# Kernel tuning notes

Measured on AMD Instinct MI355X. Metric: run time of the kernel, lower is better.

Reference implementation:

```python
import jax, jax.numpy as jnp
import numpy as np

D_MODEL = 256
NUM_ITEMS = 16
TOPK = 4
TAU = 0.1
EPS = 1e-12  # torch F.normalize eps


def _l2norm(x):
    n = jnp.sqrt(jnp.sum(x * x, axis=-1, keepdims=True))
    return x / jnp.maximum(n, EPS)


def setup_inputs() -> dict:
    key = jax.random.key(0)
    kq, km = jax.random.split(key)
    queries = jax.random.normal(kq, (32, 4096, D_MODEL), dtype=jnp.float32)
    memory = jax.random.normal(km, (NUM_ITEMS, D_MODEL), dtype=jnp.float32)
    memory = _l2norm(memory)  # init normalizes the bank to unit vectors
    return {"queries": queries, "memory": memory}


def reference(queries, memory):
    # queries: [B, Np, d]; memory: [M, d]
    q = _l2norm(queries)
    m = _l2norm(memory)
    sim = jnp.einsum('bnd,md->bnm', q, m) / TAU            # [B, Np, M]
    topk_sim, topk_idx = jax.lax.top_k(sim, TOPK)          # [B, Np, k]
    topk_w = jax.nn.softmax(topk_sim, axis=-1)             # [B, Np, k]
    mem_sel = memory[topk_idx]                             # [B, Np, k, d] (raw memory, matching torch)
    retrieved = jnp.einsum('bnk,bnkd->bnd', topk_w, mem_sel)
    sim_max = jnp.max(sim, axis=-1, keepdims=True)         # [B, Np, 1]
    return retrieved, sim_max
```

## Files before the change

### kernel.cpp

```cpp
#include <hip/hip_runtime.h>
#include <math.h>

#define D 256
#define M 16
#define TAU 0.1f
#define EPSN 1e-12f
#define MEM_STRIDE 260
#define NWAVES 4
#define BATCH 16
#define ROWS_PER_BLOCK (NWAVES * BATCH)

template <int CTRL, int ROW_MASK, int BANK_MASK>
__device__ __forceinline__ float dpp_add(float x) {
    int xi = __builtin_bit_cast(int, x);
    int mi = __builtin_amdgcn_update_dpp(0, xi, CTRL, ROW_MASK, BANK_MASK, true);
    return x + __builtin_bit_cast(float, mi);
}
__device__ __forceinline__ float wave_sum(float x) {
    x = dpp_add<0x111, 0xf, 0xf>(x);
    x = dpp_add<0x112, 0xf, 0xf>(x);
    x = dpp_add<0x114, 0xf, 0xe>(x);
    x = dpp_add<0x118, 0xf, 0xc>(x);
    x = dpp_add<0x142, 0xa, 0xf>(x);
    x = dpp_add<0x143, 0xc, 0xf>(x);
    int t = __builtin_amdgcn_readlane(__builtin_bit_cast(int, x), 63);
    return __builtin_bit_cast(float, t);
}

__global__ __launch_bounds__(256, 4)
void epm_kernel(const float* __restrict__ q, const float* __restrict__ mem,
                float* __restrict__ ret_out, float* __restrict__ smax_out)
{
    __shared__ __align__(16) float mem_lds[M * MEM_STRIDE];
    __shared__ float inv_nm_lds[M];
    __shared__ __align__(16) float qbuf[NWAVES][4 * 68];
    __shared__ float simbuf[NWAVES][M * 17];
    __shared__ float nbuf[NWAVES][BATCH];
    __shared__ __align__(16) float wbuf[NWAVES][BATCH * 4];
    __shared__ int   mbuf[NWAVES][BATCH];

    const int tid  = threadIdx.x;
    const int wv   = tid >> 6;
    const int lane = tid & 63;
    const int m    = lane & 15;
    const int c    = lane >> 4;

    {
        const float4* m4 = (const float4*)mem;
        #pragma unroll
        for (int p = 0; p < 4; ++p) {
            int vi  = p * 256 + tid;
            int row = vi >> 6;
            int col = (vi & 63) * 4;
            float4 v = m4[vi];
            *(float4*)&mem_lds[row * MEM_STRIDE + col] = v;
        }
    }
    __syncthreads();

    if (tid < M) {
        const float4* r4 = (const float4*)&mem_lds[tid * MEM_STRIDE];
        float ss = 0.f;
        #pragma unroll
        for (int j = 0; j < D / 4; ++j) {
            float4 v = r4[j];
            ss += v.x * v.x + v.y * v.y + v.z * v.z + v.w * v.w;
        }
        inv_nm_lds[tid] = 1.0f / fmaxf(sqrtf(ss), EPSN);
    }
    __syncthreads();

    float4 memr[16];
    {
        const float4* src = (const float4*)&mem_lds[m * MEM_STRIDE + c * 64];
        #pragma unroll
        for (int j = 0; j < 16; ++j) memr[j] = src[j];
    }
    const float scale_m = inv_nm_lds[m] * (1.0f / TAU);

    const int wave_row0 = blockIdx.x * ROWS_PER_BLOCK + wv * BATCH;
    float* myq = &qbuf[wv][0];
    float* simw = &simbuf[wv][0];

    float4 qv = ((const float4*)q)[(size_t)wave_row0 * 64 + lane];
    #pragma unroll
    for (int r = 0; r < BATCH; ++r) {
        float4 qn = qv;
        if (r + 1 < BATCH)
            qn = ((const float4*)q)[(size_t)(wave_row0 + r + 1) * 64 + lane];

        float sq = qv.x * qv.x + qv.y * qv.y + qv.z * qv.z + qv.w * qv.w;
        float ss = wave_sum(sq);
        if (lane == 0) nbuf[wv][r] = ss;

        *(float4*)&myq[(lane >> 4) * 68 + (lane & 15) * 4] = qv;

        float acc = 0.f;
        const float4* qs = (const float4*)&myq[c * 68];
        #pragma unroll
        for (int j = 0; j < 16; ++j) {
            float4 a = qs[j];
            float4 b = memr[j];
            acc += a.x * b.x + a.y * b.y + a.z * b.z + a.w * b.w;
        }
        acc += __shfl_xor(acc, 16);
        acc += __shfl_xor(acc, 32);
        if (c == 0) simw[m * 17 + r] = acc * scale_m;
        qv = qn;
    }

    if (lane < BATCH) {
        const int r = lane;
        float ssq = nbuf[wv][r];
        float inv_nq = 1.0f / fmaxf(sqrtf(ssq), EPSN);

        float k0 = -INFINITY, k1 = -INFINITY, k2 = -INFINITY, k3 = -INFINITY;
        #pragma unroll
        for (int mm = 0; mm < M; ++mm) {
            float s = simw[mm * 17 + r] * inv_nq;
            int si = (__builtin_bit_cast(int, s) & ~15) | (15 - mm);
            float ks = __builtin_bit_cast(float, si);
            bool g0 = ks > k0, g1 = ks > k1, g2 = ks > k2, g3 = ks > k3;
            float n3 = g2 ? k2 : (g3 ? ks : k3);
            float n2 = g1 ? k1 : (g2 ? ks : k2);
            float n1 = g0 ? k0 : (g1 ? ks : k1);
            float n0 = g0 ? ks : k0;
            k0 = n0; k1 = n1; k2 = n2; k3 = n3;
        }
        int m0 = 15 - (__builtin_bit_cast(int, k0) & 15);
        int m1 = 15 - (__builtin_bit_cast(int, k1) & 15);
        int m2 = 15 - (__builtin_bit_cast(int, k2) & 15);
        int m3 = 15 - (__builtin_bit_cast(int, k3) & 15);

        float w0 = 1.0f;
        float w1 = __expf(k1 - k0);
        float w2 = __expf(k2 - k0);
        float w3 = __expf(k3 - k0);
        float invd = 1.0f / (w0 + w1 + w2 + w3);

        *(float4*)&wbuf[wv][r * 4] = make_float4(w0 * invd, w1 * invd, w2 * invd, w3 * invd);
        mbuf[wv][r] = m0 | (m1 << 8) | (m2 << 16) | (m3 << 24);

        smax_out[wave_row0 + r] = k0;
    }

    #pragma unroll
    for (int r = 0; r < BATCH; ++r) {
        float4 w = *(const float4*)&wbuf[wv][r * 4];
        int mp = mbuf[wv][r];
        float4 accv = make_float4(0.f, 0.f, 0.f, 0.f);
        #pragma unroll
        for (int k = 0; k < 4; ++k) {
            int mk = (mp >> (8 * k)) & 15;
            float wk = (k == 0) ? w.x : (k == 1) ? w.y : (k == 2) ? w.z : w.w;
            float4 mv = *(const float4*)&mem_lds[mk * MEM_STRIDE + 4 * lane];
            accv.x += wk * mv.x; accv.y += wk * mv.y;
            accv.z += wk * mv.z; accv.w += wk * mv.w;
        }
        ((float4*)ret_out)[(size_t)(wave_row0 + r) * 64 + lane] = accv;
    }
}

extern "C" void kernel_launch(void* const* d_in, const int* in_sizes, int n_in,
                              void* d_out, int out_size, void* d_ws, size_t ws_size,
                              hipStream_t stream) {
    const float* queries = (const float*)d_in[0];
    const float* memory  = (const float*)d_in[1];
    float* out = (float*)d_out;

    const int rows = in_sizes[0] / D;
    float* ret_out  = out;
    float* smax_out = out + (size_t)rows * D;

    const int blocks = rows / ROWS_PER_BLOCK;
    epm_kernel<<<blocks, 64 * NWAVES, 0, stream>>>(queries, memory, ret_out, smax_out);
}
```

Baseline: 241.7 us.

## Compute similarities with per-lane memory slices and butterfly mux reduction

Each lane now holds a 4-float slice of all 16 memory rows in registers and computes partial dot products for all items, then reduces them with a transpose-style butterfly shuffle (mux_reduce), dropping the LDS staging of each query. Memory norms are computed the same way instead of by a 16-thread serial loop, which removes one block barrier. The query prefetch depth goes from 1 to 4 rows. This trades LDS traffic and barriers for more shuffles and register pressure (16 float4 plus 4 prefetched float4).

```diff
diff --git a/kernel.cpp b/kernel.cpp
--- a/kernel.cpp
+++ b/kernel.cpp
@@ -3,12 +3,17 @@
 
 #define D 256
 #define M 16
-#define TAU 0.1f
+#define INV_TAU 10.0f
 #define EPSN 1e-12f
 #define MEM_STRIDE 260
 #define NWAVES 4
 #define BATCH 16
 #define ROWS_PER_BLOCK (NWAVES * BATCH)
+#define SIMW_STRIDE 20
+
+__device__ __forceinline__ float dot4(float4 a, float4 b) {
+    return a.x * b.x + a.y * b.y + a.z * b.z + a.w * b.w;
+}
 
 template <int CTRL, int ROW_MASK, int BANK_MASK>
 __device__ __forceinline__ float dpp_add(float x) {
@@ -27,14 +32,52 @@
     return __builtin_bit_cast(float, t);
 }
 
+__device__ __forceinline__ float mux_reduce(float vals[16], int lane) {
+    {
+        const bool b = (lane & 1) != 0;
+        #pragma unroll
+        for (int j = 0; j < 8; ++j) {
+            float send = b ? vals[j] : vals[j + 8];
+            float recv = __shfl_xor(send, 1);
+            vals[j] = (b ? vals[j + 8] : vals[j]) + recv;
+        }
+    }
+    {
+        const bool b = (lane & 2) != 0;
+        #pragma unroll
+        for (int j = 0; j < 4; ++j) {
+            float send = b ? vals[j] : vals[j + 4];
+            float recv = __shfl_xor(send, 2);
+            vals[j] = (b ? vals[j + 4] : vals[j]) + recv;
+        }
+    }
+    {
+        const bool b = (lane & 4) != 0;
+        #pragma unroll
+        for (int j = 0; j < 2; ++j) {
+            float send = b ? vals[j] : vals[j + 2];
+            float recv = __shfl_xor(send, 4);
+            vals[j] = (b ? vals[j + 2] : vals[j]) + recv;
+        }
+    }
+    {
+        const bool b = (lane & 8) != 0;
+        float send = b ? vals[0] : vals[1];
+        float recv = __shfl_xor(send, 8);
+        vals[0] = (b ? vals[1] : vals[0]) + recv;
+    }
+    float v = vals[0];
+    v += __shfl_xor(v, 16);
+    v += __shfl_xor(v, 32);
+    return v;
+}
+
 __global__ __launch_bounds__(256, 4)
 void epm_kernel(const float* __restrict__ q, const float* __restrict__ mem,
                 float* __restrict__ ret_out, float* __restrict__ smax_out)
 {
     __shared__ __align__(16) float mem_lds[M * MEM_STRIDE];
-    __shared__ float inv_nm_lds[M];
-    __shared__ __align__(16) float qbuf[NWAVES][4 * 68];
-    __shared__ float simbuf[NWAVES][M * 17];
+    __shared__ __align__(16) float simbuf[NWAVES][BATCH * SIMW_STRIDE];
     __shared__ float nbuf[NWAVES][BATCH];
     __shared__ __align__(16) float wbuf[NWAVES][BATCH * 4];
     __shared__ int   mbuf[NWAVES][BATCH];
@@ -42,8 +85,11 @@
     const int tid  = threadIdx.x;
     const int wv   = tid >> 6;
     const int lane = tid & 63;
-    const int m    = lane & 15;
-    const int c    = lane >> 4;
+
+    float4 memr2[16];
+    #pragma unroll
+    for (int m = 0; m < M; ++m)
+        memr2[m] = *(const float4*)&mem[m * D + 4 * lane];
 
     {
         const float4* m4 = (const float4*)mem;
@@ -58,55 +104,43 @@
     }
     __syncthreads();
 
-    if (tid < M) {
-        const float4* r4 = (const float4*)&mem_lds[tid * MEM_STRIDE];
-        float ss = 0.f;
-        #pragma unroll
-        for (int j = 0; j < D / 4; ++j) {
-            float4 v = r4[j];
-            ss += v.x * v.x + v.y * v.y + v.z * v.z + v.w * v.w;
-        }
-        inv_nm_lds[tid] = 1.0f / fmaxf(sqrtf(ss), EPSN);
-    }
-    __syncthreads();
-
-    float4 memr[16];
-    {
-        const float4* src = (const float4*)&mem_lds[m * MEM_STRIDE + c * 64];
-        #pragma unroll
-        for (int j = 0; j < 16; ++j) memr[j] = src[j];
-    }
-    const float scale_m = inv_nm_lds[m] * (1.0f / TAU);
+    float invm_l;
+    {
+        float nmv[16];
+        #pragma unroll
+        for (int m = 0; m < M; ++m) nmv[m] = dot4(memr2[m], memr2[m]);
+        float nm = mux_reduce(nmv, lane);
+        invm_l = 1.0f / fmaxf(sqrtf(nm), EPSN);
+    }
+
+    const int brl = ((lane & 1) << 3) | ((lane & 2) << 1)
+                  | ((lane & 4) >> 1) | ((lane & 8) >> 3);
 
     const int wave_row0 = blockIdx.x * ROWS_PER_BLOCK + wv * BATCH;
-    float* myq = &qbuf[wv][0];
     float* simw = &simbuf[wv][0];
-
-    float4 qv = ((const float4*)q)[(size_t)wave_row0 * 64 + lane];
+    const float4* q4 = (const float4*)q;
+
+    float4 qpre[4];
+    #pragma unroll
+    for (int r = 0; r < 4; ++r)
+        qpre[r] = q4[(size_t)(wave_row0 + r) * 64 + lane];
+
     #pragma unroll
     for (int r = 0; r < BATCH; ++r) {
-        float4 qn = qv;
-        if (r + 1 < BATCH)
-            qn = ((const float4*)q)[(size_t)(wave_row0 + r + 1) * 64 + lane];
-
-        float sq = qv.x * qv.x + qv.y * qv.y + qv.z * qv.z + qv.w * qv.w;
-        float ss = wave_sum(sq);
-        if (lane == 0) nbuf[wv][r] = ss;
-
-        *(float4*)&myq[(lane >> 4) * 68 + (lane & 15) * 4] = qv;
-
-        float acc = 0.f;
-        const float4* qs = (const float4*)&myq[c * 68];
-        #pragma unroll
-        for (int j = 0; j < 16; ++j) {
-            float4 a = qs[j];
-            float4 b = memr[j];
-            acc += a.x * b.x + a.y * b.y + a.z * b.z + a.w * b.w;
-        }
-        acc += __shfl_xor(acc, 16);
-        acc += __shfl_xor(acc, 32);
-        if (c == 0) simw[m * 17 + r] = acc * scale_m;
-        qv = qn;
+        float4 qv = qpre[r & 3];
+        if (r + 4 < BATCH)
+            qpre[r & 3] = q4[(size_t)(wave_row0 + r + 4) * 64 + lane];
+
+        float sq = wave_sum(dot4(qv, qv));
+        if (lane == 0) nbuf[wv][r] = sq;
+
+        float vals[16];
+        #pragma unroll
+        for (int m = 0; m < M; ++m) vals[m] = dot4(qv, memr2[m]);
+
+        float v = mux_reduce(vals, lane);
+
+        if (lane < 16) simw[r * SIMW_STRIDE + brl] = v * invm_l * INV_TAU;
     }
 
     if (lane < BATCH) {
@@ -117,7 +151,7 @@
         float k0 = -INFINITY, k1 = -INFINITY, k2 = -INFINITY, k3 = -INFINITY;
         #pragma unroll
         for (int mm = 0; mm < M; ++mm) {
-            float s = simw[mm * 17 + r] * inv_nq;
+            float s = simw[r * SIMW_STRIDE + mm] * inv_nq;
             int si = (__builtin_bit_cast(int, s) & ~15) | (15 - mm);
             float ks = __builtin_bit_cast(float, si);
             bool g0 = ks > k0, g1 = ks > k1, g2 = ks > k2, g3 = ks > k3;
```

Measured after the change: 241.7 us. No clear change (+0.0%).
